# Optimization experiments

Hardware: AMD Instinct MI355X
Metric: run time of the kernel (lower is better)

Reference implementation:

```python
import jax, jax.numpy as jnp
import numpy as np

N_HEADS = 8
D_K = 64
SCALE = D_K ** (-0.5)


def setup_inputs() -> dict:
    key = jax.random.key(0)
    k1, k2, k3 = jax.random.split(key, 3)
    B, C, H, W = 8, 512, 32, 32
    x = jax.random.normal(k1, (B, C, H, W), dtype=jnp.float32)
    # Linear weights stored as [in, out] so y = x @ W + b (same math as torch Linear)
    W_qkv = jax.random.normal(k2, (C, N_HEADS * D_K * 3), dtype=jnp.float32) * (1.0 / np.sqrt(C))
    b_qkv = jnp.zeros((N_HEADS * D_K * 3,), dtype=jnp.float32)
    W_out = jax.random.normal(k3, (N_HEADS * D_K, C), dtype=jnp.float32) * (1.0 / np.sqrt(N_HEADS * D_K))
    b_out = jnp.zeros((C,), dtype=jnp.float32)
    return {"x": x, "W_qkv": W_qkv, "b_qkv": b_qkv, "W_out": W_out, "b_out": b_out}


def reference(x, W_qkv, b_qkv, W_out, b_out):
    B, C, H, W = x.shape
    N = H * W
    # [B, C, H, W] -> [B, N, C]  (tokens are spatial positions)
    xf = jnp.transpose(x.reshape(B, C, N), (0, 2, 1))
    # NOTE: the original forward never applies self.norm, so neither do we.
    qkv = xf @ W_qkv + b_qkv                       # [B, N, 3*h*d]
    qkv = qkv.reshape(B, N, N_HEADS, 3 * D_K)
    q, k, v = jnp.split(qkv, 3, axis=-1)           # each [B, N, h, d]
    attn = jnp.einsum('bihd,bjhd->bijh', q, k) * SCALE
    attn = jax.nn.softmax(attn, axis=2)            # softmax over key index j
    res = jnp.einsum('bijh,bjhd->bihd', attn, v)   # [B, N, h, d]
    res = res.reshape(B, N, N_HEADS * D_K)
    res = res @ W_out + b_out
    res = res + xf                                 # residual
    res = jnp.transpose(res, (0, 2, 1)).reshape(B, C, H, W)
    return res
```

## Files before the change

### kernel.cpp

```cpp
#include <hip/hip_runtime.h>
#include <hip/hip_bf16.h>
#include <cstdint>

typedef __bf16 bf16;
typedef __attribute__((ext_vector_type(8))) __bf16 bf16x8;
typedef __attribute__((ext_vector_type(4))) __bf16 bf16x4;
typedef __attribute__((ext_vector_type(4))) float f32x4;

#define CEXP 0.1803368801111244f

__global__ __launch_bounds__(256) void xpose_k(const float* __restrict__ x,
                                               bf16* __restrict__ xT) {
  __shared__ bf16 t[32][33];
  const int b = blockIdx.z;
  const float* src = x + (size_t)b * 512 * 1024;
  bf16* dst = xT + (size_t)b * 1024 * 512;
  const int c0 = blockIdx.x * 32, r0 = blockIdx.y * 32;
  const int tx = threadIdx.x, ty = threadIdx.y;
#pragma unroll
  for (int i = 0; i < 4; ++i)
    t[ty + i * 8][tx] = (bf16)src[(size_t)(r0 + ty + i * 8) * 1024 + c0 + tx];
  __syncthreads();
#pragma unroll
  for (int i = 0; i < 4; ++i)
    dst[(size_t)(c0 + ty + i * 8) * 512 + r0 + tx] = t[tx][ty + i * 8];
}

__global__ __launch_bounds__(256) void prep_k(const float* __restrict__ Wqkv,
                                              const float* __restrict__ Wout,
                                              bf16* __restrict__ WqkvT,
                                              bf16* __restrict__ WoutT) {
  __shared__ bf16 t[32][33];
  const int z = blockIdx.z;
  const float* src;
  bf16* dst;
  int R, C;
  if (z == 0) {
    src = Wqkv; dst = WqkvT; R = 512; C = 1536;
  } else {
    if (blockIdx.x >= 16) return;
    src = Wout; dst = WoutT; R = 512; C = 512;
  }
  const int c0 = blockIdx.x * 32, r0 = blockIdx.y * 32;
  const int tx = threadIdx.x, ty = threadIdx.y;
#pragma unroll
  for (int i = 0; i < 4; ++i)
    t[ty + i * 8][tx] = (bf16)src[(size_t)(r0 + ty + i * 8) * C + c0 + tx];
  __syncthreads();
#pragma unroll
  for (int i = 0; i < 4; ++i)
    dst[(size_t)(c0 + ty + i * 8) * R + r0 + tx] = t[tx][ty + i * 8];
}

__global__ __launch_bounds__(256) void gemm_qkv(const bf16* __restrict__ xT,
                                                const bf16* __restrict__ WqkvT,
                                                const float* __restrict__ bqkv,
                                                bf16* __restrict__ Qb,
                                                bf16* __restrict__ Kb,
                                                bf16* __restrict__ Vb) {
  __shared__ bf16 As[128 * 72];
  __shared__ bf16 Bs[128 * 72];
  const int b = blockIdx.z;
  const int m0 = blockIdx.y * 128;
  const int co0 = blockIdx.x * 128;
  const int tid = threadIdx.x;
  const int w = tid >> 6, l = tid & 63;
  const int wr = w >> 1, wc = w & 1;
  const int quad = l >> 4, l16 = l & 15;

  const bf16* A = xT + (size_t)b * 1024 * 512;

  f32x4 acc[4][4];
#pragma unroll
  for (int i = 0; i < 4; ++i)
#pragma unroll
    for (int j = 0; j < 4; ++j) acc[i][j] = (f32x4){0.f, 0.f, 0.f, 0.f};

  const int srow = w * 32 + (l >> 3);
  const int scol = (l & 7) * 8;

  for (int kk = 0; kk < 8; ++kk) {
    const int k0 = kk * 64;
    bf16x8 av[4], bv[4];
#pragma unroll
    for (int i = 0; i < 4; ++i) {
      av[i] = *(const bf16x8*)&A[(size_t)(m0 + srow + i * 8) * 512 + k0 + scol];
      bv[i] = *(const bf16x8*)&WqkvT[(size_t)(co0 + srow + i * 8) * 512 + k0 + scol];
    }
#pragma unroll
    for (int i = 0; i < 4; ++i) {
      *(bf16x8*)&As[(srow + i * 8) * 72 + scol] = av[i];
      *(bf16x8*)&Bs[(srow + i * 8) * 72 + scol] = bv[i];
    }
    __syncthreads();
#pragma unroll
    for (int ks = 0; ks < 2; ++ks) {
      bf16x8 a[4], bb[4];
#pragma unroll
      for (int rb = 0; rb < 4; ++rb)
        a[rb] = *(const bf16x8*)&As[(wr * 64 + rb * 16 + l16) * 72 + ks * 32 + quad * 8];
#pragma unroll
      for (int cb = 0; cb < 4; ++cb)
        bb[cb] = *(const bf16x8*)&Bs[(wc * 64 + cb * 16 + l16) * 72 + ks * 32 + quad * 8];
#pragma unroll
      for (int rb = 0; rb < 4; ++rb)
#pragma unroll
        for (int cb = 0; cb < 4; ++cb)
          acc[rb][cb] = __builtin_amdgcn_mfma_f32_16x16x32_bf16(a[rb], bb[cb], acc[rb][cb], 0, 0, 0);
    }
    __syncthreads();
  }

#pragma unroll
  for (int cb = 0; cb < 4; ++cb) {
    const int co = co0 + wc * 64 + cb * 16 + l16;
    const int h = co / 192;
    const int rem = co - h * 192;
    const int part = rem >> 6;
    const int dd = rem & 63;
    const float bias = bqkv[co];
    if (part == 2) {
      bf16* base = Vb + ((size_t)(b * 8 + h) * 64 + dd) * 1024;
#pragma unroll
      for (int rb = 0; rb < 4; ++rb) {
        const int n = m0 + wr * 64 + rb * 16 + quad * 4;
        f32x4 v = acc[rb][cb];
        bf16x4 ov;
#pragma unroll
        for (int r = 0; r < 4; ++r) ov[r] = (bf16)(v[r] + bias);
        *(bf16x4*)&base[n] = ov;
      }
    } else {
      const float sc = (part == 0) ? CEXP : 1.0f;
      bf16* dst = (part == 0) ? Qb : Kb;
      bf16* base = dst + ((size_t)(b * 8 + h) * 1024) * 64 + dd;
#pragma unroll
      for (int rb = 0; rb < 4; ++rb) {
        const int n = m0 + wr * 64 + rb * 16 + quad * 4;
        f32x4 v = acc[rb][cb];
#pragma unroll
        for (int r = 0; r < 4; ++r) base[(size_t)(n + r) * 64] = (bf16)((v[r] + bias) * sc);
      }
    }
  }
}

__global__ __launch_bounds__(256) void attn_k(const bf16* __restrict__ Qb,
                                              const bf16* __restrict__ Kb,
                                              const bf16* __restrict__ Vb,
                                              bf16* __restrict__ Ob) {
  __shared__ bf16 Ks[128 * 72];
  __shared__ bf16 Vs[64 * 136];
  __shared__ bf16 PQs[128 * 136];
  const int bh = blockIdx.x;
  const int b = bh >> 3, h = bh & 7;
  const int q0 = blockIdx.y * 128;
  const int tid = threadIdx.x;
  const int w = tid >> 6, l = tid & 63;
  const int quad = l >> 4, l16 = l & 15;

  const bf16* Qg = Qb + (size_t)bh * 1024 * 64;
  const bf16* Kg = Kb + (size_t)bh * 1024 * 64;
  const bf16* Vg = Vb + (size_t)bh * 64 * 1024;

  {
    const int r = tid >> 1, c = (tid & 1) * 32;
#pragma unroll
    for (int e = 0; e < 4; ++e)
      *(bf16x8*)&PQs[r * 72 + c + e * 8] =
          *(const bf16x8*)&Qg[(size_t)(q0 + r) * 64 + c + e * 8];
  }
  __syncthreads();
  bf16x8 qb[8][2];
#pragma unroll
  for (int nb = 0; nb < 8; ++nb)
#pragma unroll
    for (int ks = 0; ks < 2; ++ks)
      qb[nb][ks] = *(const bf16x8*)&PQs[(nb * 16 + l16) * 72 + ks * 32 + quad * 8];

  bf16x8 ones;
#pragma unroll
  for (int e = 0; e < 8; ++e) ones[e] = (bf16)1.0f;

  f32x4 o[2][4], acc_l[2];
#pragma unroll
  for (int mt = 0; mt < 2; ++mt) {
    acc_l[mt] = (f32x4){0.f, 0.f, 0.f, 0.f};
#pragma unroll
    for (int db = 0; db < 4; ++db) o[mt][db] = (f32x4){0.f, 0.f, 0.f, 0.f};
  }

  const int kr = tid >> 1, kc = (tid & 1) * 32;
  const int vr = tid >> 2, vc = (tid & 3) * 32;

  bf16x8 ka[4], va[4];
#pragma unroll
  for (int e = 0; e < 4; ++e) {
    ka[e] = *(const bf16x8*)&Kg[(size_t)kr * 64 + kc + e * 8];
    va[e] = *(const bf16x8*)&Vg[(size_t)vr * 1024 + vc + e * 8];
  }

  for (int kv = 0; kv < 8; ++kv) {
    __syncthreads();
#pragma unroll
    for (int e = 0; e < 4; ++e) {
      *(bf16x8*)&Ks[kr * 72 + kc + e * 8] = ka[e];
      *(bf16x8*)&Vs[vr * 136 + vc + e * 8] = va[e];
    }
    __syncthreads();
    if (kv < 7) {
      const int j0 = (kv + 1) * 128;
#pragma unroll
      for (int e = 0; e < 4; ++e) {
        ka[e] = *(const bf16x8*)&Kg[(size_t)(j0 + kr) * 64 + kc + e * 8];
        va[e] = *(const bf16x8*)&Vg[(size_t)vr * 1024 + j0 + vc + e * 8];
      }
    }

    f32x4 s[8][2];
#pragma unroll
    for (int nb = 0; nb < 8; ++nb)
#pragma unroll
      for (int jb = 0; jb < 2; ++jb) s[nb][jb] = (f32x4){0.f, 0.f, 0.f, 0.f};
#pragma unroll
    for (int ks = 0; ks < 2; ++ks) {
      bf16x8 kaf[2];
#pragma unroll
      for (int jb = 0; jb < 2; ++jb)
        kaf[jb] = *(const bf16x8*)&Ks[(w * 32 + jb * 16 + l16) * 72 + ks * 32 + quad * 8];
#pragma unroll
      for (int nb = 0; nb < 8; ++nb)
#pragma unroll
        for (int jb = 0; jb < 2; ++jb)
          s[nb][jb] = __builtin_amdgcn_mfma_f32_16x16x32_bf16(kaf[jb], qb[nb][ks], s[nb][jb], 0, 0, 0);
    }

#pragma unroll
    for (int nb = 0; nb < 8; ++nb)
#pragma unroll
      for (int jb = 0; jb < 2; ++jb) {
        bf16x4 pk;
#pragma unroll
        for (int rr = 0; rr < 4; ++rr) pk[rr] = (bf16)__builtin_amdgcn_exp2f(s[nb][jb][rr]);
        *(bf16x4*)&PQs[(nb * 16 + l16) * 136 + w * 32 + jb * 16 + quad * 4] = pk;
      }
    __syncthreads();

#pragma unroll
    for (int kj = 0; kj < 4; ++kj) {
      bf16x8 ap[2];
#pragma unroll
      for (int mt = 0; mt < 2; ++mt) {
        ap[mt] = *(const bf16x8*)&PQs[(w * 32 + mt * 16 + l16) * 136 + kj * 32 + quad * 8];
        acc_l[mt] = __builtin_amdgcn_mfma_f32_16x16x32_bf16(ap[mt], ones, acc_l[mt], 0, 0, 0);
      }
#pragma unroll
      for (int db = 0; db < 4; ++db) {
        bf16x8 bv = *(const bf16x8*)&Vs[(db * 16 + l16) * 136 + kj * 32 + quad * 8];
#pragma unroll
        for (int mt = 0; mt < 2; ++mt)
          o[mt][db] = __builtin_amdgcn_mfma_f32_16x16x32_bf16(ap[mt], bv, o[mt][db], 0, 0, 0);
      }
    }
  }

  bf16* Og = Ob + (size_t)b * 1024 * 512 + h * 64;
#pragma unroll
  for (int mt = 0; mt < 2; ++mt) {
    f32x4 inv;
#pragma unroll
    for (int rr = 0; rr < 4; ++rr) inv[rr] = 1.0f / acc_l[mt][rr];
#pragma unroll
    for (int db = 0; db < 4; ++db)
#pragma unroll
      for (int rr = 0; rr < 4; ++rr) {
        const int n = q0 + w * 32 + mt * 16 + quad * 4 + rr;
        Og[(size_t)n * 512 + db * 16 + l16] = (bf16)(o[mt][db][rr] * inv[rr]);
      }
  }
}

__global__ __launch_bounds__(256) void gemm_out(const bf16* __restrict__ Ob,
                                                const bf16* __restrict__ WoutT,
                                                const float* __restrict__ bout,
                                                const float* __restrict__ x,
                                                float* __restrict__ out) {
  __shared__ bf16 As[128 * 72];
  __shared__ bf16 Bs[64 * 72];
  const int b = blockIdx.z;
  const int m0 = blockIdx.y * 128;
  const int co0 = blockIdx.x * 64;
  const int tid = threadIdx.x;
  const int w = tid >> 6, l = tid & 63;
  const int wr = w >> 1, wc = w & 1;
  const int quad = l >> 4, l16 = l & 15;

  const bf16* A = Ob + (size_t)b * 1024 * 512;

  f32x4 acc[4][2];
#pragma unroll
  for (int i = 0; i < 4; ++i)
#pragma unroll
    for (int j = 0; j < 2; ++j) acc[i][j] = (f32x4){0.f, 0.f, 0.f, 0.f};

  const int srow = w * 32 + (l >> 3);
  const int scol = (l & 7) * 8;
  const int brow = tid >> 2;
  const int bcol = (tid & 3) * 16;

  for (int kk = 0; kk < 8; ++kk) {
    const int k0 = kk * 64;
    bf16x8 av[4], bv[2];
#pragma unroll
    for (int i = 0; i < 4; ++i)
      av[i] = *(const bf16x8*)&A[(size_t)(m0 + srow + i * 8) * 512 + k0 + scol];
#pragma unroll
    for (int i = 0; i < 2; ++i)
      bv[i] = *(const bf16x8*)&WoutT[(size_t)(co0 + brow) * 512 + k0 + bcol + i * 8];
#pragma unroll
    for (int i = 0; i < 4; ++i)
      *(bf16x8*)&As[(srow + i * 8) * 72 + scol] = av[i];
#pragma unroll
    for (int i = 0; i < 2; ++i)
      *(bf16x8*)&Bs[brow * 72 + bcol + i * 8] = bv[i];
    __syncthreads();
#pragma unroll
    for (int ks = 0; ks < 2; ++ks) {
      bf16x8 a[4], bb[2];
#pragma unroll
      for (int rb = 0; rb < 4; ++rb)
        a[rb] = *(const bf16x8*)&As[(wr * 64 + rb * 16 + l16) * 72 + ks * 32 + quad * 8];
#pragma unroll
      for (int cb = 0; cb < 2; ++cb)
        bb[cb] = *(const bf16x8*)&Bs[(wc * 32 + cb * 16 + l16) * 72 + ks * 32 + quad * 8];
#pragma unroll
      for (int rb = 0; rb < 4; ++rb)
#pragma unroll
        for (int cb = 0; cb < 2; ++cb)
          acc[rb][cb] = __builtin_amdgcn_mfma_f32_16x16x32_bf16(a[rb], bb[cb], acc[rb][cb], 0, 0, 0);
    }
    __syncthreads();
  }

#pragma unroll
  for (int cb = 0; cb < 2; ++cb) {
    const int c = co0 + wc * 32 + cb * 16 + l16;
    const float bias = bout[c];
#pragma unroll
    for (int rb = 0; rb < 4; ++rb) {
      const int n = m0 + wr * 64 + rb * 16 + quad * 4;
      const size_t off = ((size_t)b * 512 + c) * 1024 + n;
      f32x4 res = *(const f32x4*)&x[off];
      f32x4 v = acc[rb][cb];
      f32x4 ov;
#pragma unroll
      for (int r = 0; r < 4; ++r) ov[r] = v[r] + bias + res[r];
      *(f32x4*)&out[off] = ov;
    }
  }
}

extern "C" void kernel_launch(void* const* d_in, const int* in_sizes, int n_in,
                              void* d_out, int out_size, void* d_ws, size_t ws_size,
                              hipStream_t stream) {
  const float* x = (const float*)d_in[0];
  const float* Wqkv = (const float*)d_in[1];
  const float* bqkv = (const float*)d_in[2];
  const float* Wout = (const float*)d_in[3];
  const float* bout = (const float*)d_in[4];
  float* out = (float*)d_out;
  char* ws = (char*)d_ws;

  const size_t MB = 1024 * 1024;
  bf16* xT = (bf16*)(ws);
  bf16* Ob = xT;
  bf16* Qbuf = (bf16*)(ws + 8 * MB);
  bf16* Kbuf = (bf16*)(ws + 16 * MB);
  bf16* Vbuf = (bf16*)(ws + 24 * MB);
  bf16* WqkvT = (bf16*)(ws + 32 * MB);
  bf16* WoutT = (bf16*)(ws + 32 * MB + 1572864);
  if (ws_size < 32 * MB + 1572864 + 524288) return;

  xpose_k<<<dim3(32, 16, 8), dim3(32, 8), 0, stream>>>(x, xT);
  prep_k<<<dim3(48, 16, 2), dim3(32, 8), 0, stream>>>(Wqkv, Wout, WqkvT, WoutT);
  gemm_qkv<<<dim3(12, 8, 8), 256, 0, stream>>>(xT, WqkvT, bqkv, Qbuf, Kbuf, Vbuf);
  attn_k<<<dim3(64, 8), 256, 0, stream>>>(Qbuf, Kbuf, Vbuf, Ob);
  gemm_out<<<dim3(8, 8, 8), 256, 0, stream>>>(Ob, WoutT, bout, x, out);
}
```

Before: 148.3 us.

## Keep attention probabilities in registers and merge transpose prep kernels

The attention kernel now gives each wave its own 32 query rows. The exponentiated scores stay in registers and feed the PV MFMA directly as the A operand, which removes the shared P buffer, its writes, and one barrier per KV tile. V fragments are gathered with a permuted k-index so they match the register layout of the score accumulators. Q is loaded straight from global memory. The x transpose and weight transposes are also merged into a single launch. In exchange, each wave now recomputes QK against the full 128-key tile, which adds register pressure from the larger score and K fragment arrays.

Result: no change. 145.6 us (-1.8%).

```diff
diff --git a/kernel.cpp b/kernel.cpp
--- a/kernel.cpp
+++ b/kernel.cpp
@@ -9,37 +9,27 @@
 
 #define CEXP 0.1803368801111244f
 
-__global__ __launch_bounds__(256) void xpose_k(const float* __restrict__ x,
-                                               bf16* __restrict__ xT) {
-  __shared__ bf16 t[32][33];
-  const int b = blockIdx.z;
-  const float* src = x + (size_t)b * 512 * 1024;
-  bf16* dst = xT + (size_t)b * 1024 * 512;
-  const int c0 = blockIdx.x * 32, r0 = blockIdx.y * 32;
-  const int tx = threadIdx.x, ty = threadIdx.y;
-#pragma unroll
-  for (int i = 0; i < 4; ++i)
-    t[ty + i * 8][tx] = (bf16)src[(size_t)(r0 + ty + i * 8) * 1024 + c0 + tx];
-  __syncthreads();
-#pragma unroll
-  for (int i = 0; i < 4; ++i)
-    dst[(size_t)(c0 + ty + i * 8) * 512 + r0 + tx] = t[tx][ty + i * 8];
-}
-
-__global__ __launch_bounds__(256) void prep_k(const float* __restrict__ Wqkv,
-                                              const float* __restrict__ Wout,
-                                              bf16* __restrict__ WqkvT,
-                                              bf16* __restrict__ WoutT) {
+__global__ __launch_bounds__(256) void prep_all(const float* __restrict__ x,
+                                                const float* __restrict__ Wqkv,
+                                                const float* __restrict__ Wout,
+                                                bf16* __restrict__ xT,
+                                                bf16* __restrict__ WqkvT,
+                                                bf16* __restrict__ WoutT) {
   __shared__ bf16 t[32][33];
   const int z = blockIdx.z;
   const float* src;
   bf16* dst;
-  int R, C;
-  if (z == 0) {
-    src = Wqkv; dst = WqkvT; R = 512; C = 1536;
+  int C;
+  if (z < 8) {
+    if (blockIdx.x >= 32) return;
+    src = x + (size_t)z * 512 * 1024;
+    dst = xT + (size_t)z * 1024 * 512;
+    C = 1024;
+  } else if (z == 8) {
+    src = Wqkv; dst = WqkvT; C = 1536;
   } else {
     if (blockIdx.x >= 16) return;
-    src = Wout; dst = WoutT; R = 512; C = 512;
+    src = Wout; dst = WoutT; C = 512;
   }
   const int c0 = blockIdx.x * 32, r0 = blockIdx.y * 32;
   const int tx = threadIdx.x, ty = threadIdx.y;
@@ -49,7 +39,7 @@
   __syncthreads();
 #pragma unroll
   for (int i = 0; i < 4; ++i)
-    dst[(size_t)(c0 + ty + i * 8) * R + r0 + tx] = t[tx][ty + i * 8];
+    dst[(size_t)(c0 + ty + i * 8) * 512 + r0 + tx] = t[tx][ty + i * 8];
 }
 
 __global__ __launch_bounds__(256) void gemm_qkv(const bf16* __restrict__ xT,
@@ -151,7 +141,6 @@
                                               bf16* __restrict__ Ob) {
   __shared__ bf16 Ks[128 * 72];
   __shared__ bf16 Vs[64 * 136];
-  __shared__ bf16 PQs[128 * 136];
   const int bh = blockIdx.x;
   const int b = bh >> 3, h = bh & 7;
   const int q0 = blockIdx.y * 128;
@@ -163,20 +152,12 @@
   const bf16* Kg = Kb + (size_t)bh * 1024 * 64;
   const bf16* Vg = Vb + (size_t)bh * 64 * 1024;
 
-  {
-    const int r = tid >> 1, c = (tid & 1) * 32;
-#pragma unroll
-    for (int e = 0; e < 4; ++e)
-      *(bf16x8*)&PQs[r * 72 + c + e * 8] =
-          *(const bf16x8*)&Qg[(size_t)(q0 + r) * 64 + c + e * 8];
-  }
-  __syncthreads();
-  bf16x8 qb[8][2];
-#pragma unroll
-  for (int nb = 0; nb < 8; ++nb)
+  bf16x8 qb[2][2];
+#pragma unroll
+  for (int mt = 0; mt < 2; ++mt)
 #pragma unroll
     for (int ks = 0; ks < 2; ++ks)
-      qb[nb][ks] = *(const bf16x8*)&PQs[(nb * 16 + l16) * 72 + ks * 32 + quad * 8];
+      qb[mt][ks] = *(const bf16x8*)&Qg[(size_t)(q0 + w * 32 + mt * 16 + l16) * 64 + ks * 32 + quad * 8];
 
   bf16x8 ones;
 #pragma unroll
@@ -217,49 +198,49 @@
       }
     }
 
-    f32x4 s[8][2];
-#pragma unroll
-    for (int nb = 0; nb < 8; ++nb)
-#pragma unroll
-      for (int jb = 0; jb < 2; ++jb) s[nb][jb] = (f32x4){0.f, 0.f, 0.f, 0.f};
+    f32x4 s[2][8];
+#pragma unroll
+    for (int mt = 0; mt < 2; ++mt)
+#pragma unroll
+      for (int jb = 0; jb < 8; ++jb) s[mt][jb] = (f32x4){0.f, 0.f, 0.f, 0.f};
 #pragma unroll
     for (int ks = 0; ks < 2; ++ks) {
-      bf16x8 kaf[2];
-#pragma unroll
-      for (int jb = 0; jb < 2; ++jb)
-        kaf[jb] = *(const bf16x8*)&Ks[(w * 32 + jb * 16 + l16) * 72 + ks * 32 + quad * 8];
-#pragma unroll
-      for (int nb = 0; nb < 8; ++nb)
-#pragma unroll
-        for (int jb = 0; jb < 2; ++jb)
-          s[nb][jb] = __builtin_amdgcn_mfma_f32_16x16x32_bf16(kaf[jb], qb[nb][ks], s[nb][jb], 0, 0, 0);
-    }
-
-#pragma unroll
-    for (int nb = 0; nb < 8; ++nb)
-#pragma unroll
-      for (int jb = 0; jb < 2; ++jb) {
-        bf16x4 pk;
-#pragma unroll
-        for (int rr = 0; rr < 4; ++rr) pk[rr] = (bf16)__builtin_amdgcn_exp2f(s[nb][jb][rr]);
-        *(bf16x4*)&PQs[(nb * 16 + l16) * 136 + w * 32 + jb * 16 + quad * 4] = pk;
-      }
-    __syncthreads();
+      bf16x8 kaf[8];
+#pragma unroll
+      for (int jb = 0; jb < 8; ++jb)
+        kaf[jb] = *(const bf16x8*)&Ks[(jb * 16 + l16) * 72 + ks * 32 + quad * 8];
+#pragma unroll
+      for (int jb = 0; jb < 8; ++jb)
+#pragma unroll
+        for (int mt = 0; mt < 2; ++mt)
+          s[mt][jb] = __builtin_amdgcn_mfma_f32_16x16x32_bf16(kaf[jb], qb[mt][ks], s[mt][jb], 0, 0, 0);
+    }
 
 #pragma unroll
     for (int kj = 0; kj < 4; ++kj) {
-      bf16x8 ap[2];
+      bf16x8 bv[4];
+#pragma unroll
+      for (int db = 0; db < 4; ++db) {
+        const bf16x4 lo = *(const bf16x4*)&Vs[(db * 16 + l16) * 136 + kj * 32 + quad * 4];
+        const bf16x4 hi = *(const bf16x4*)&Vs[(db * 16 + l16) * 136 + kj * 32 + 16 + quad * 4];
+#pragma unroll
+        for (int e = 0; e < 4; ++e) {
+          bv[db][e] = lo[e];
+          bv[db][4 + e] = hi[e];
+        }
+      }
 #pragma unroll
       for (int mt = 0; mt < 2; ++mt) {
-        ap[mt] = *(const bf16x8*)&PQs[(w * 32 + mt * 16 + l16) * 136 + kj * 32 + quad * 8];
-        acc_l[mt] = __builtin_amdgcn_mfma_f32_16x16x32_bf16(ap[mt], ones, acc_l[mt], 0, 0, 0);
-      }
-#pragma unroll
-      for (int db = 0; db < 4; ++db) {
-        bf16x8 bv = *(const bf16x8*)&Vs[(db * 16 + l16) * 136 + kj * 32 + quad * 8];
-#pragma unroll
-        for (int mt = 0; mt < 2; ++mt)
-          o[mt][db] = __builtin_amdgcn_mfma_f32_16x16x32_bf16(ap[mt], bv, o[mt][db], 0, 0, 0);
+        bf16x8 ap;
+#pragma unroll
+        for (int rr = 0; rr < 4; ++rr) {
+          ap[rr] = (bf16)__builtin_amdgcn_exp2f(s[mt][2 * kj][rr]);
+          ap[4 + rr] = (bf16)__builtin_amdgcn_exp2f(s[mt][2 * kj + 1][rr]);
+        }
+        acc_l[mt] = __builtin_amdgcn_mfma_f32_16x16x32_bf16(ap, ones, acc_l[mt], 0, 0, 0);
+#pragma unroll
+        for (int db = 0; db < 4; ++db)
+          o[mt][db] = __builtin_amdgcn_mfma_f32_16x16x32_bf16(ap, bv[db], o[mt][db], 0, 0, 0);
       }
     }
   }
@@ -381,8 +362,7 @@
   bf16* WoutT = (bf16*)(ws + 32 * MB + 1572864);
   if (ws_size < 32 * MB + 1572864 + 524288) return;
 
-  xpose_k<<<dim3(32, 16, 8), dim3(32, 8), 0, stream>>>(x, xT);
-  prep_k<<<dim3(48, 16, 2), dim3(32, 8), 0, stream>>>(Wqkv, Wout, WqkvT, WoutT);
+  prep_all<<<dim3(48, 16, 10), dim3(32, 8), 0, stream>>>(x, Wqkv, Wout, xT, WqkvT, WoutT);
   gemm_qkv<<<dim3(12, 8, 8), 256, 0, stream>>>(xT, WqkvT, bqkv, Qbuf, Kbuf, Vbuf);
   attn_k<<<dim3(64, 8), 256, 0, stream>>>(Qbuf, Kbuf, Vbuf, Ob);
   gemm_out<<<dim3(8, 8, 8), 256, 0, stream>>>(Ob, WoutT, bout, x, out);
```
